# Kernel tuning notes

Measured on AMD Instinct MI355X. Metric: run time of the kernel, lower is better.

## Reference

```python
import jax, jax.numpy as jnp
import numpy as np

B, H, S, DK = 4, 16, 2048, 64


def setup_inputs() -> dict:
    key = jax.random.key(0)
    kq, kk, kv, km = jax.random.split(key, 4)
    Q = jax.random.normal(kq, (B, H, S, DK), dtype=jnp.float32)
    K = jax.random.normal(kk, (B, H, S, DK), dtype=jnp.float32)
    V = jax.random.normal(kv, (B, H, S, DK), dtype=jnp.float32)
    mask = (jax.random.uniform(km, (B, 1, S, S)) > 0.1).astype(jnp.float32)
    return {"Q": Q, "K": K, "V": V, "mask": mask}


def reference(Q, K, V, mask):
    d_k = Q.shape[-1]
    # unnormalized exp scores (no max subtraction), multiplicative mask
    scores = jnp.exp(jnp.einsum("bhqd,bhkd->bhqk", Q, K) / jnp.sqrt(jnp.float32(d_k)))
    scores = scores * mask
    attn = scores / (jnp.sum(scores, axis=-1, keepdims=True) + 1e-8)
    return jnp.einsum("bhqk,bhkd->bhqd", attn, V)
```

## Files before the change

### kernel.cpp

```cpp
#include <hip/hip_runtime.h>

namespace {
constexpr int S  = 2048;
constexpr int D  = 64;
constexpr int BQ = 256;
constexpr int BK = 64;
constexpr int NT = 512;
constexpr int NKT = S / BK;

typedef short bf16x8 __attribute__((ext_vector_type(8)));
typedef float f32x4  __attribute__((ext_vector_type(4)));

__device__ inline unsigned short bf16c(float x) {
  __bf16 h = (__bf16)x;
  return __builtin_bit_cast(unsigned short, h);
}
__device__ inline unsigned pk2(float a, float b) {
  return (unsigned)bf16c(a) | ((unsigned)bf16c(b) << 16);
}
__device__ inline void gld_lds16(const void* g, void* l) {
  __builtin_amdgcn_global_load_lds(
      (const __attribute__((address_space(1))) unsigned int*)g,
      (__attribute__((address_space(3))) unsigned int*)l, 16, 0, 0);
}
#if __has_builtin(__builtin_amdgcn_exp2f)
__device__ inline float exp2v(float x) { return __builtin_amdgcn_exp2f(x); }
#else
__device__ inline float exp2v(float x) { return __expf(x * 0.6931471805599453f); }
#endif

__device__ inline int kswz_of_row(int row) {
  return (row & 3) | (((row >> 3) & 1) << 2);
}

__device__ inline bf16x8 mk_pa(f32x4 s0, f32x4 s1, unsigned mw0, unsigned mw1) {
  float p0 = exp2v(s0[0]) * (float)(mw0 & 0xffu);
  float p1 = exp2v(s0[1]) * (float)((mw0 >> 8) & 0xffu);
  float p2 = exp2v(s0[2]) * (float)((mw0 >> 16) & 0xffu);
  float p3 = exp2v(s0[3]) * (float)(mw0 >> 24);
  float p4 = exp2v(s1[0]) * (float)(mw1 & 0xffu);
  float p5 = exp2v(s1[1]) * (float)((mw1 >> 8) & 0xffu);
  float p6 = exp2v(s1[2]) * (float)((mw1 >> 16) & 0xffu);
  float p7 = exp2v(s1[3]) * (float)(mw1 >> 24);
  uint4 u = make_uint4(pk2(p0, p1), pk2(p2, p3), pk2(p4, p5), pk2(p6, p7));
  return __builtin_bit_cast(bf16x8, u);
}

__global__ __launch_bounds__(256) void prep_k(const float* __restrict__ K,
                                              unsigned short* __restrict__ Kws) {
  int gid = blockIdx.x * 256 + threadIdx.x;
  int row = gid >> 3;
  int g   = gid & 7;
  const float* src = K + (size_t)row * 64 + g * 8;
  float4 a = *(const float4*)src;
  float4 b = *(const float4*)(src + 4);
  uint4 w;
  w.x = pk2(a.x, a.y); w.y = pk2(a.z, a.w);
  w.z = pk2(b.x, b.y); w.w = pk2(b.z, b.w);
  *(uint4*)(Kws + (size_t)row * 64 + ((g ^ kswz_of_row(row)) * 8)) = w;
}

__global__ __launch_bounds__(256) void prep_v(const float* __restrict__ V,
                                              unsigned short* __restrict__ Vws) {
  __shared__ float tl[64 * 68];
  const int t = threadIdx.x;
  const size_t tile = blockIdx.x;
  const float* src = V + tile * (64 * 64);
#pragma unroll
  for (int rep = 0; rep < 4; ++rep) {
    int idx = t + rep * 256;
    int row = idx >> 4, d4 = idx & 15;
    float4 v = *(const float4*)(src + row * 64 + d4 * 4);
    *(float4*)(tl + row * 68 + d4 * 4) = v;
  }
  __syncthreads();
  unsigned short* dstT = Vws + tile * (64 * 64);
#pragma unroll
  for (int rep = 0; rep < 2; ++rep) {
    int d  = (t & 31) + rep * 32;
    int kg = t >> 5;
    float x[8];
#pragma unroll
    for (int j = 0; j < 8; ++j) x[j] = tl[(kg * 8 + j) * 68 + d];
    uint4 w;
    w.x = pk2(x[0], x[1]); w.y = pk2(x[2], x[3]);
    w.z = pk2(x[4], x[5]); w.w = pk2(x[6], x[7]);
    *(uint4*)(dstT + d * 64 + ((kg ^ (d & 7)) * 8)) = w;
  }
}

__global__ __launch_bounds__(512) void prep_m(const float* __restrict__ M,
                                              unsigned char* __restrict__ M2) {
  __shared__ unsigned nibs[32][129];
  const int t  = threadIdx.x;
  const int b  = blockIdx.x >> 6;
  const int qg = blockIdx.x & 63;
  const float* src = M + ((size_t)b * S + (size_t)qg * 32) * S;

#pragma unroll
  for (int pass = 0; pass < 8; ++pass) {
    int idx = pass * 512 + t;
    int q  = idx >> 7;
    int kc = idx & 127;
    const float* p = src + (size_t)q * S + kc * 16;
    unsigned w = 0;
#pragma unroll
    for (int j = 0; j < 4; ++j) {
      float4 v = *(const float4*)(p + j * 4);
      unsigned nib = (v.x != 0.f ? 1u : 0u) | (v.y != 0.f ? 2u : 0u) |
                     (v.z != 0.f ? 4u : 0u) | (v.w != 0.f ? 8u : 0u);
      w |= nib << (8 * j);
    }
    nibs[q][kc] = w;
  }
  __syncthreads();

  const int e    = t & 127;
  const int lane = e >> 1, g = e & 1;
  const int n16  = lane & 15, quad = lane >> 4;
  const int qq   = g * 16 + n16;
  const int c    = quad >> 1;
  const int sh0  = 8 * ((2 * quad) & 3);
  unsigned char* dstb = M2 + ((size_t)b * NKT * 64 + qg) * 2048 + (size_t)e * 16;
#pragma unroll
  for (int i = 0; i < 8; ++i) {
    int kt = (t >> 7) + i * 4;
    unsigned d0 = nibs[qq][kt * 4 + c];
    unsigned d1 = nibs[qq][kt * 4 + 2 + c];
    unsigned n00 = (d0 >> sh0) & 0xFu;
    unsigned n01 = (d0 >> (sh0 + 8)) & 0xFu;
    unsigned n10 = (d1 >> sh0) & 0xFu;
    unsigned n11 = (d1 >> (sh0 + 8)) & 0xFu;
    uint4 out;
    out.x = (n00 * 0x00204081u) & 0x01010101u;
    out.y = (n01 * 0x00204081u) & 0x01010101u;
    out.z = (n10 * 0x00204081u) & 0x01010101u;
    out.w = (n11 * 0x00204081u) & 0x01010101u;
    *(uint4*)(dstb + (size_t)kt * (64 * 64 * 32)) = out;
  }
}

__global__ __launch_bounds__(NT, 4)
void attn3(const float* __restrict__ Qg, const unsigned char* __restrict__ M2,
           const unsigned short* __restrict__ Kws,
           const unsigned short* __restrict__ Vws,
           float* __restrict__ Og) {
  __shared__ __align__(16) unsigned short sK[2][BK * D];
  __shared__ __align__(16) unsigned short sV[2][BK * D];

  const int t    = threadIdx.x;
  const int wave = t >> 6;
  const int lane = t & 63;
  const int quad = lane >> 4;
  const int n16  = lane & 15;

  const int bh = blockIdx.y;
  const int b  = bh >> 4;
  const int q0 = blockIdx.x * BQ;
  const int qg = blockIdx.x * 8 + wave;

  const unsigned short* Kb = Kws + (size_t)bh * S * D;
  const unsigned short* Vb = Vws + (size_t)bh * S * D;
  const unsigned char* Mp = M2 + (((size_t)b * NKT * 64 + qg) * 64 + lane) * 32;
  constexpr size_t MKT = (size_t)64 * 64 * 32;

  const int h2 = n16 >> 2, rr = n16 & 3;
  const int krow0 = (8 * h2 + rr) * 64;

  const int sw = n16 & 7;
  const int ga = (quad ^ sw) * 8;
  const int gb = ((quad + 4) ^ sw) * 8;

  constexpr float QS = 0.18033688011112042f;
  const float* QbA = Qg + ((size_t)bh * S + q0 + wave * 32 + n16) * D;
  bf16x8 aqA[2], aqB[2];
#pragma unroll
  for (int ks = 0; ks < 2; ++ks) {
    const float* qp = QbA + ks * 32 + quad * 8;
    float4 x = *(const float4*)qp;
    float4 y = *(const float4*)(qp + 4);
    bf16x8 a;
    a[0] = (short)bf16c(x.x * QS); a[1] = (short)bf16c(x.y * QS);
    a[2] = (short)bf16c(x.z * QS); a[3] = (short)bf16c(x.w * QS);
    a[4] = (short)bf16c(y.x * QS); a[5] = (short)bf16c(y.y * QS);
    a[6] = (short)bf16c(y.z * QS); a[7] = (short)bf16c(y.w * QS);
    aqA[ks] = a;
    const float* qp2 = qp + 16 * D;
    float4 x2 = *(const float4*)qp2;
    float4 y2 = *(const float4*)(qp2 + 4);
    bf16x8 a2;
    a2[0] = (short)bf16c(x2.x * QS); a2[1] = (short)bf16c(x2.y * QS);
    a2[2] = (short)bf16c(x2.z * QS); a2[3] = (short)bf16c(x2.w * QS);
    a2[4] = (short)bf16c(y2.x * QS); a2[5] = (short)bf16c(y2.y * QS);
    a2[6] = (short)bf16c(y2.z * QS); a2[7] = (short)bf16c(y2.w * QS);
    aqB[ks] = a2;
  }

  bf16x8 ones;
#pragma unroll
  for (int i = 0; i < 8; ++i) ones[i] = (short)0x3F80;

  f32x4 oA[4], oB[4];
#pragma unroll
  for (int nt = 0; nt < 4; ++nt) {
    oA[nt] = (f32x4){0.f, 0.f, 0.f, 0.f};
    oB[nt] = (f32x4){0.f, 0.f, 0.f, 0.f};
  }
  f32x4 rsA = (f32x4){0.f, 0.f, 0.f, 0.f};
  f32x4 rsB = (f32x4){0.f, 0.f, 0.f, 0.f};

  gld_lds16(Kb + wave * 512 + lane * 8, &sK[0][wave * 512]);
  gld_lds16(Vb + wave * 512 + lane * 8, &sV[0][wave * 512]);

#pragma unroll 2
  for (int kt = 0; kt < NKT; ++kt) {
    const int cur = kt & 1, nxt = cur ^ 1;
    __syncthreads();

    uint4 mkA = *(const uint4*)(Mp + (size_t)kt * MKT);
    uint4 mkB = *(const uint4*)(Mp + (size_t)kt * MKT + 16);

    if (kt + 1 < NKT) {
      gld_lds16(Kb + (size_t)(kt + 1) * (BK * D) + wave * 512 + lane * 8,
                &sK[nxt][wave * 512]);
      gld_lds16(Vb + (size_t)(kt + 1) * (BK * D) + wave * 512 + lane * 8,
                &sV[nxt][wave * 512]);
    }

    bf16x8 paA[2], paB[2];
#pragma unroll
    for (int ks = 0; ks < 2; ++ks) {
      const unsigned short* base = &sK[cur][krow0 + ks * 2048];
      bf16x8 k0a = *(const bf16x8*)(base + ga);
      bf16x8 k0b = *(const bf16x8*)(base + gb);
      bf16x8 k1a = *(const bf16x8*)(base + 256 + ga);
      bf16x8 k1b = *(const bf16x8*)(base + 256 + gb);
      const f32x4 z = (f32x4){0.f, 0.f, 0.f, 0.f};

      f32x4 sA0 = __builtin_amdgcn_mfma_f32_16x16x32_bf16(k0a, aqA[0], z, 0, 0, 0);
      sA0 = __builtin_amdgcn_mfma_f32_16x16x32_bf16(k0b, aqA[1], sA0, 0, 0, 0);
      f32x4 sA1 = __builtin_amdgcn_mfma_f32_16x16x32_bf16(k1a, aqA[0], z, 0, 0, 0);
      sA1 = __builtin_amdgcn_mfma_f32_16x16x32_bf16(k1b, aqA[1], sA1, 0, 0, 0);
      paA[ks] = mk_pa(sA0, sA1, ks ? mkA.z : mkA.x, ks ? mkA.w : mkA.y);

      f32x4 sB0 = __builtin_amdgcn_mfma_f32_16x16x32_bf16(k0a, aqB[0], z, 0, 0, 0);
      sB0 = __builtin_amdgcn_mfma_f32_16x16x32_bf16(k0b, aqB[1], sB0, 0, 0, 0);
      f32x4 sB1 = __builtin_amdgcn_mfma_f32_16x16x32_bf16(k1a, aqB[0], z, 0, 0, 0);
      sB1 = __builtin_amdgcn_mfma_f32_16x16x32_bf16(k1b, aqB[1], sB1, 0, 0, 0);
      paB[ks] = mk_pa(sB0, sB1, ks ? mkB.z : mkB.x, ks ? mkB.w : mkB.y);
    }

    rsA = __builtin_amdgcn_mfma_f32_16x16x32_bf16(ones, paA[0], rsA, 0, 0, 0);
    rsA = __builtin_amdgcn_mfma_f32_16x16x32_bf16(ones, paA[1], rsA, 0, 0, 0);
    rsB = __builtin_amdgcn_mfma_f32_16x16x32_bf16(ones, paB[0], rsB, 0, 0, 0);
    rsB = __builtin_amdgcn_mfma_f32_16x16x32_bf16(ones, paB[1], rsB, 0, 0, 0);

#pragma unroll
    for (int nt = 0; nt < 4; ++nt) {
      const int row = nt * 16 + n16;
      bf16x8 v0 = *(const bf16x8*)(sV[cur] + row * 64 + ga);
      bf16x8 v1 = *(const bf16x8*)(sV[cur] + row * 64 + gb);
      oA[nt] = __builtin_amdgcn_mfma_f32_16x16x32_bf16(v0, paA[0], oA[nt], 0, 0, 0);
      oA[nt] = __builtin_amdgcn_mfma_f32_16x16x32_bf16(v1, paA[1], oA[nt], 0, 0, 0);
      oB[nt] = __builtin_amdgcn_mfma_f32_16x16x32_bf16(v0, paB[0], oB[nt], 0, 0, 0);
      oB[nt] = __builtin_amdgcn_mfma_f32_16x16x32_bf16(v1, paB[1], oB[nt], 0, 0, 0);
    }
  }

  const float invA = 1.0f / (rsA[0] + 1e-8f);
  const float invB = 1.0f / (rsB[0] + 1e-8f);
  float* OA = Og + ((size_t)bh * S + q0 + wave * 32 + n16) * D;
#pragma unroll
  for (int nt = 0; nt < 4; ++nt) {
    float4 wa = make_float4(oA[nt][0] * invA, oA[nt][1] * invA,
                            oA[nt][2] * invA, oA[nt][3] * invA);
    *(float4*)(OA + nt * 16 + quad * 4) = wa;
    float4 wb = make_float4(oB[nt][0] * invB, oB[nt][1] * invB,
                            oB[nt][2] * invB, oB[nt][3] * invB);
    *(float4*)(OA + 16 * D + nt * 16 + quad * 4) = wb;
  }
}
}

extern "C" void kernel_launch(void* const* d_in, const int* in_sizes, int n_in,
                              void* d_out, int out_size, void* d_ws, size_t ws_size,
                              hipStream_t stream) {
  const float* Q = (const float*)d_in[0];
  const float* K = (const float*)d_in[1];
  const float* V = (const float*)d_in[2];
  const float* M = (const float*)d_in[3];
  float* O = (float*)d_out;

  unsigned short* Kws = (unsigned short*)d_ws;
  unsigned short* Vws = Kws + (size_t)64 * S * D;
  unsigned char*  M2  = (unsigned char*)(Vws + (size_t)64 * S * D);

  prep_k<<<dim3(64 * S * D / 8 / 256), 256, 0, stream>>>(K, Kws);
  prep_v<<<dim3(64 * NKT), 256, 0, stream>>>(V, Vws);
  prep_m<<<dim3(4 * 64), 512, 0, stream>>>(M, M2);
  attn3<<<dim3(S / BQ, 64), NT, 0, stream>>>(Q, M2, Kws, Vws, O);
}
```

Baseline: 270.3 us.

## Merge prep kernels into one launch, prefetch mask words, raise MFMA priority

The three preprocessing kernels (K bf16 conversion, V transpose, mask packing) become a single kernel that branches on block index, removing two launches and letting the three jobs run side by side. The V path now stages its transposed output in shared memory and writes it out with contiguous 16-byte stores. The attention loop loads the mask words for the next key tile one iteration early, double-buffered in registers, and raises wave priority around the MFMA section with s_setprio. In exchange the fused prep kernel reserves 51 KB of shared memory per block, which may lower occupancy for the K and mask branches, and the loop holds more live registers.

```diff
diff --git a/kernel.cpp b/kernel.cpp
--- a/kernel.cpp
+++ b/kernel.cpp
@@ -46,97 +46,105 @@
   return __builtin_bit_cast(bf16x8, u);
 }
 
-__global__ __launch_bounds__(256) void prep_k(const float* __restrict__ K,
-                                              unsigned short* __restrict__ Kws) {
-  int gid = blockIdx.x * 256 + threadIdx.x;
-  int row = gid >> 3;
-  int g   = gid & 7;
-  const float* src = K + (size_t)row * 64 + g * 8;
-  float4 a = *(const float4*)src;
-  float4 b = *(const float4*)(src + 4);
-  uint4 w;
-  w.x = pk2(a.x, a.y); w.y = pk2(a.z, a.w);
-  w.z = pk2(b.x, b.y); w.w = pk2(b.z, b.w);
-  *(uint4*)(Kws + (size_t)row * 64 + ((g ^ kswz_of_row(row)) * 8)) = w;
-}
-
-__global__ __launch_bounds__(256) void prep_v(const float* __restrict__ V,
-                                              unsigned short* __restrict__ Vws) {
-  __shared__ float tl[64 * 68];
-  const int t = threadIdx.x;
-  const size_t tile = blockIdx.x;
-  const float* src = V + tile * (64 * 64);
-#pragma unroll
-  for (int rep = 0; rep < 4; ++rep) {
-    int idx = t + rep * 256;
-    int row = idx >> 4, d4 = idx & 15;
-    float4 v = *(const float4*)(src + row * 64 + d4 * 4);
-    *(float4*)(tl + row * 68 + d4 * 4) = v;
-  }
-  __syncthreads();
-  unsigned short* dstT = Vws + tile * (64 * 64);
-#pragma unroll
-  for (int rep = 0; rep < 2; ++rep) {
-    int d  = (t & 31) + rep * 32;
-    int kg = t >> 5;
-    float x[8];
-#pragma unroll
-    for (int j = 0; j < 8; ++j) x[j] = tl[(kg * 8 + j) * 68 + d];
+__global__ __launch_bounds__(512) void prep_all(
+    const float* __restrict__ K, const float* __restrict__ V,
+    const float* __restrict__ M, unsigned short* __restrict__ Kws,
+    unsigned short* __restrict__ Vws, unsigned char* __restrict__ M2) {
+  __shared__ __align__(16) unsigned char smem[51200];
+  const int blk = blockIdx.x;
+  const int t   = threadIdx.x;
+
+  if (blk < 2048) {
+    int gid = blk * 512 + t;
+    int row = gid >> 3;
+    int g   = gid & 7;
+    const float* src = K + (size_t)row * 64 + g * 8;
+    float4 a = *(const float4*)src;
+    float4 b = *(const float4*)(src + 4);
     uint4 w;
-    w.x = pk2(x[0], x[1]); w.y = pk2(x[2], x[3]);
-    w.z = pk2(x[4], x[5]); w.w = pk2(x[6], x[7]);
-    *(uint4*)(dstT + d * 64 + ((kg ^ (d & 7)) * 8)) = w;
-  }
-}
-
-__global__ __launch_bounds__(512) void prep_m(const float* __restrict__ M,
-                                              unsigned char* __restrict__ M2) {
-  __shared__ unsigned nibs[32][129];
-  const int t  = threadIdx.x;
-  const int b  = blockIdx.x >> 6;
-  const int qg = blockIdx.x & 63;
-  const float* src = M + ((size_t)b * S + (size_t)qg * 32) * S;
-
-#pragma unroll
-  for (int pass = 0; pass < 8; ++pass) {
-    int idx = pass * 512 + t;
-    int q  = idx >> 7;
-    int kc = idx & 127;
-    const float* p = src + (size_t)q * S + kc * 16;
-    unsigned w = 0;
-#pragma unroll
-    for (int j = 0; j < 4; ++j) {
-      float4 v = *(const float4*)(p + j * 4);
-      unsigned nib = (v.x != 0.f ? 1u : 0u) | (v.y != 0.f ? 2u : 0u) |
-                     (v.z != 0.f ? 4u : 0u) | (v.w != 0.f ? 8u : 0u);
-      w |= nib << (8 * j);
-    }
-    nibs[q][kc] = w;
-  }
-  __syncthreads();
-
-  const int e    = t & 127;
-  const int lane = e >> 1, g = e & 1;
-  const int n16  = lane & 15, quad = lane >> 4;
-  const int qq   = g * 16 + n16;
-  const int c    = quad >> 1;
-  const int sh0  = 8 * ((2 * quad) & 3);
-  unsigned char* dstb = M2 + ((size_t)b * NKT * 64 + qg) * 2048 + (size_t)e * 16;
-#pragma unroll
-  for (int i = 0; i < 8; ++i) {
-    int kt = (t >> 7) + i * 4;
-    unsigned d0 = nibs[qq][kt * 4 + c];
-    unsigned d1 = nibs[qq][kt * 4 + 2 + c];
-    unsigned n00 = (d0 >> sh0) & 0xFu;
-    unsigned n01 = (d0 >> (sh0 + 8)) & 0xFu;
-    unsigned n10 = (d1 >> sh0) & 0xFu;
-    unsigned n11 = (d1 >> (sh0 + 8)) & 0xFu;
-    uint4 out;
-    out.x = (n00 * 0x00204081u) & 0x01010101u;
-    out.y = (n01 * 0x00204081u) & 0x01010101u;
-    out.z = (n10 * 0x00204081u) & 0x01010101u;
-    out.w = (n11 * 0x00204081u) & 0x01010101u;
-    *(uint4*)(dstb + (size_t)kt * (64 * 64 * 32)) = out;
+    w.x = pk2(a.x, a.y); w.y = pk2(a.z, a.w);
+    w.z = pk2(b.x, b.y); w.w = pk2(b.z, b.w);
+    *(uint4*)(Kws + (size_t)row * 64 + ((g ^ kswz_of_row(row)) * 8)) = w;
+  } else if (blk < 3072) {
+    const int half = t >> 8;
+    const int tsub = t & 255;
+    const size_t tile = (size_t)(blk - 2048) * 2 + half;
+    float* tl = (float*)smem + half * (64 * 68);
+    unsigned short* so = (unsigned short*)(smem + 34816) + half * 4096;
+    const float* src = V + tile * (64 * 64);
+#pragma unroll
+    for (int rep = 0; rep < 4; ++rep) {
+      int idx = tsub + rep * 256;
+      int row = idx >> 4, d4 = idx & 15;
+      float4 v = *(const float4*)(src + row * 64 + d4 * 4);
+      *(float4*)(tl + row * 68 + d4 * 4) = v;
+    }
+    __syncthreads();
+#pragma unroll
+    for (int rep = 0; rep < 2; ++rep) {
+      int d  = (tsub & 31) + rep * 32;
+      int kg = tsub >> 5;
+      float x[8];
+#pragma unroll
+      for (int j = 0; j < 8; ++j) x[j] = tl[(kg * 8 + j) * 68 + d];
+      uint4 w;
+      w.x = pk2(x[0], x[1]); w.y = pk2(x[2], x[3]);
+      w.z = pk2(x[4], x[5]); w.w = pk2(x[6], x[7]);
+      *(uint4*)(so + d * 64 + ((kg ^ (d & 7)) * 8)) = w;
+    }
+    __syncthreads();
+    unsigned short* dstT = Vws + tile * (64 * 64);
+#pragma unroll
+    for (int rep = 0; rep < 2; ++rep) {
+      int i = tsub + rep * 256;
+      *(uint4*)(dstT + i * 8) = *(const uint4*)(so + i * 8);
+    }
+  } else {
+    unsigned (*nibs)[129] = (unsigned (*)[129])smem;
+    const int bqg = blk - 3072;
+    const int b  = bqg >> 6;
+    const int qg = bqg & 63;
+    const float* src = M + ((size_t)b * S + (size_t)qg * 32) * S;
+#pragma unroll
+    for (int pass = 0; pass < 8; ++pass) {
+      int idx = pass * 512 + t;
+      int q  = idx >> 7;
+      int kc = idx & 127;
+      const float* p = src + (size_t)q * S + kc * 16;
+      unsigned w = 0;
+#pragma unroll
+      for (int j = 0; j < 4; ++j) {
+        float4 v = *(const float4*)(p + j * 4);
+        unsigned nib = (v.x != 0.f ? 1u : 0u) | (v.y != 0.f ? 2u : 0u) |
+                       (v.z != 0.f ? 4u : 0u) | (v.w != 0.f ? 8u : 0u);
+        w |= nib << (8 * j);
+      }
+      nibs[q][kc] = w;
+    }
+    __syncthreads();
+    const int e    = t & 127;
+    const int lane = e >> 1, g = e & 1;
+    const int n16  = lane & 15, quad = lane >> 4;
+    const int qq   = g * 16 + n16;
+    const int c    = quad >> 1;
+    const int sh0  = 8 * ((2 * quad) & 3);
+    unsigned char* dstb = M2 + ((size_t)b * NKT * 64 + qg) * 2048 + (size_t)e * 16;
+#pragma unroll
+    for (int i = 0; i < 8; ++i) {
+      int kt = (t >> 7) + i * 4;
+      unsigned d0 = nibs[qq][kt * 4 + c];
+      unsigned d1 = nibs[qq][kt * 4 + 2 + c];
+      unsigned n00 = (d0 >> sh0) & 0xFu;
+      unsigned n01 = (d0 >> (sh0 + 8)) & 0xFu;
+      unsigned n10 = (d1 >> sh0) & 0xFu;
+      unsigned n11 = (d1 >> (sh0 + 8)) & 0xFu;
+      uint4 out;
+      out.x = (n00 * 0x00204081u) & 0x01010101u;
+      out.y = (n01 * 0x00204081u) & 0x01010101u;
+      out.z = (n10 * 0x00204081u) & 0x01010101u;
+      out.w = (n11 * 0x00204081u) & 0x01010101u;
+      *(uint4*)(dstb + (size_t)kt * (64 * 64 * 32)) = out;
+    }
   }
 }
 
@@ -211,20 +219,22 @@
 
   gld_lds16(Kb + wave * 512 + lane * 8, &sK[0][wave * 512]);
   gld_lds16(Vb + wave * 512 + lane * 8, &sV[0][wave * 512]);
+  uint4 mkA[2], mkB[2];
+  mkA[0] = *(const uint4*)Mp;
+  mkB[0] = *(const uint4*)(Mp + 16);
 
 #pragma unroll 2
   for (int kt = 0; kt < NKT; ++kt) {
     const int cur = kt & 1, nxt = cur ^ 1;
     __syncthreads();
-
-    uint4 mkA = *(const uint4*)(Mp + (size_t)kt * MKT);
-    uint4 mkB = *(const uint4*)(Mp + (size_t)kt * MKT + 16);
 
     if (kt + 1 < NKT) {
       gld_lds16(Kb + (size_t)(kt + 1) * (BK * D) + wave * 512 + lane * 8,
                 &sK[nxt][wave * 512]);
       gld_lds16(Vb + (size_t)(kt + 1) * (BK * D) + wave * 512 + lane * 8,
                 &sV[nxt][wave * 512]);
+      mkA[nxt] = *(const uint4*)(Mp + (size_t)(kt + 1) * MKT);
+      mkB[nxt] = *(const uint4*)(Mp + (size_t)(kt + 1) * MKT + 16);
     }
 
     bf16x8 paA[2], paB[2];
@@ -241,15 +251,18 @@
       sA0 = __builtin_amdgcn_mfma_f32_16x16x32_bf16(k0b, aqA[1], sA0, 0, 0, 0);
       f32x4 sA1 = __builtin_amdgcn_mfma_f32_16x16x32_bf16(k1a, aqA[0], z, 0, 0, 0);
       sA1 = __builtin_amdgcn_mfma_f32_16x16x32_bf16(k1b, aqA[1], sA1, 0, 0, 0);
-      paA[ks] = mk_pa(sA0, sA1, ks ? mkA.z : mkA.x, ks ? mkA.w : mkA.y);
+      paA[ks] = mk_pa(sA0, sA1, ks ? mkA[cur].z : mkA[cur].x,
+                                ks ? mkA[cur].w : mkA[cur].y);
 
       f32x4 sB0 = __builtin_amdgcn_mfma_f32_16x16x32_bf16(k0a, aqB[0], z, 0, 0, 0);
       sB0 = __builtin_amdgcn_mfma_f32_16x16x32_bf16(k0b, aqB[1], sB0, 0, 0, 0);
       f32x4 sB1 = __builtin_amdgcn_mfma_f32_16x16x32_bf16(k1a, aqB[0], z, 0, 0, 0);
       sB1 = __builtin_amdgcn_mfma_f32_16x16x32_bf16(k1b, aqB[1], sB1, 0, 0, 0);
-      paB[ks] = mk_pa(sB0, sB1, ks ? mkB.z : mkB.x, ks ? mkB.w : mkB.y);
-    }
-
+      paB[ks] = mk_pa(sB0, sB1, ks ? mkB[cur].z : mkB[cur].x,
+                                ks ? mkB[cur].w : mkB[cur].y);
+    }
+
+    __builtin_amdgcn_s_setprio(1);
     rsA = __builtin_amdgcn_mfma_f32_16x16x32_bf16(ones, paA[0], rsA, 0, 0, 0);
     rsA = __builtin_amdgcn_mfma_f32_16x16x32_bf16(ones, paA[1], rsA, 0, 0, 0);
     rsB = __builtin_amdgcn_mfma_f32_16x16x32_bf16(ones, paB[0], rsB, 0, 0, 0);
@@ -265,6 +278,7 @@
       oB[nt] = __builtin_amdgcn_mfma_f32_16x16x32_bf16(v0, paB[0], oB[nt], 0, 0, 0);
       oB[nt] = __builtin_amdgcn_mfma_f32_16x16x32_bf16(v1, paB[1], oB[nt], 0, 0, 0);
     }
+    __builtin_amdgcn_s_setprio(0);
   }
 
   const float invA = 1.0f / (rsA[0] + 1e-8f);
@@ -295,8 +309,6 @@
   unsigned short* Vws = Kws + (size_t)64 * S * D;
   unsigned char*  M2  = (unsigned char*)(Vws + (size_t)64 * S * D);
 
-  prep_k<<<dim3(64 * S * D / 8 / 256), 256, 0, stream>>>(K, Kws);
-  prep_v<<<dim3(64 * NKT), 256, 0, stream>>>(V, Vws);
-  prep_m<<<dim3(4 * 64), 512, 0, stream>>>(M, M2);
+  prep_all<<<dim3(3328), 512, 0, stream>>>(K, V, M, Kws, Vws, M2);
   attn3<<<dim3(S / BQ, 64), NT, 0, stream>>>(Q, M2, Kws, Vws, O);
 }
```

After: 276.2 us. 2.2% more time.
